# Kernel tuning notes

Measured on AMD Instinct MI355X. Metric: run time of the kernel, lower is better.

## Reference

```python
import jax, jax.numpy as jnp
import numpy as np

EPS = 1e-5  # BatchNorm eps (torch default)
K = 16      # num_neighbors


def _bn(x, gamma, beta, axes):
    # training-mode BatchNorm (biased variance), channel axis = 1
    mu = x.mean(axes, keepdims=True)
    var = x.var(axes, keepdims=True)
    shp = [1] * x.ndim
    shp[1] = -1
    return (x - mu) * jax.lax.rsqrt(var + EPS) * gamma.reshape(shp) + beta.reshape(shp)


def setup_inputs() -> dict:
    key = jax.random.key(0)
    ks = jax.random.split(key, 6)
    B, C, N, E = 4, 3, 4096, 256
    s = lambda k_, shp, fan: jax.random.normal(k_, shp, jnp.float32) * np.float32(1.0 / np.sqrt(fan))
    return {
        "x": jax.random.normal(ks[0], (B, C, N), jnp.float32),
        "g1": jnp.ones((C,), jnp.float32), "b1": jnp.zeros((C,), jnp.float32),
        "W1": s(ks[1], (E, C), C), "bw1": jnp.zeros((E,), jnp.float32),
        "g2a": jnp.ones((C,), jnp.float32), "b2a": jnp.zeros((C,), jnp.float32),
        "W2a": s(ks[2], (E, C), C),
        "g2b": jnp.ones((E,), jnp.float32), "b2b": jnp.zeros((E,), jnp.float32),
        "W2b": s(ks[3], (E, E), E),
        "Wf": s(ks[4], (E, 2 * E), 2 * E), "bf": jnp.zeros((E,), jnp.float32),
    }


def reference(x, g1, b1, W1, bw1, g2a, b2a, W2a, g2b, b2b, W2b, Wf, bf):
    B, C, N = x.shape
    xn = _bn(x, g1, b1, (0, 2))                               # BatchNorm1d
    point_emb = jnp.einsum('ec,bcn->ben', W1, xn) + bw1[None, :, None]  # conv1 (1x1)
    # dist = -||xi - xj||; torch topk(dist, largest=False) picks the K LARGEST
    # distances. Squared distance is monotone in the norm, so top_k on d2 gives
    # identical indices without materializing [B,3,N,N].
    x2 = jnp.sum(xn * xn, axis=1)                             # [B,N]
    d2 = x2[:, :, None] + x2[:, None, :] - 2.0 * jnp.einsum('bcn,bcm->bnm', xn, xn)
    _, idx = jax.lax.top_k(d2, min(K, N))                     # [B,N,K]
    idx = idx[:, :, 1:]                                       # original loop skips index 0
    gathered = jax.vmap(lambda xb, ib: xb[:, ib])(xn, idx)    # [B,C,N,K-1]
    neigh = gathered - xn[:, :, :, None]                      # edge features
    h = _bn(neigh, g2a, b2a, (0, 2, 3))                       # BatchNorm2d(Cin)
    h = jnp.einsum('ec,bcnk->benk', W2a, h)                   # 1x1 conv, no bias
    h = jax.nn.gelu(_bn(h, g2b, b2b, (0, 2, 3)), approximate=False)
    h = jnp.einsum('fe,benk->bfnk', W2b, h)                   # 1x1 conv, no bias
    neigh_emb = h.max(-1)                                     # max over neighbors
    feat = jnp.concatenate([point_emb, neigh_emb], axis=1)    # [B,2E,N]
    return jnp.einsum('of,bfn->bon', Wf, feat) + bf[None, :, None]
```

## Files before the change

### kernel.cpp

```cpp
#include <hip/hip_runtime.h>
#include <float.h>
#include <math.h>

#define EPS 1e-5f
constexpr int B = 4, C = 3, N = 4096, E = 256;
constexpr int KNN = 15;
constexpr int BN_ = B * N;
constexpr int P = 8;
constexpr int SR  = 264;
constexpr int SRF = 520;

typedef short bf8 __attribute__((ext_vector_type(8)));
typedef float f4  __attribute__((ext_vector_type(4)));

static __device__ __forceinline__ unsigned short f2bf(float f) {
    union { float f; unsigned int u; } v; v.f = f;
    unsigned int r = v.u + 0x7FFFu + ((v.u >> 16) & 1u);
    return (unsigned short)(r >> 16);
}
static __device__ __forceinline__ unsigned int pkbf(float a, float b) {
    unsigned int r;
    asm("v_cvt_pk_bf16_f32 %0, %1, %2" : "=v"(r) : "v"(a), "v"(b));
    return r;
}
static __device__ __forceinline__ bf8 ld_bf8(const unsigned short* p) {
    return *(const bf8*)p;
}
static __device__ __forceinline__ float gelu_t(float v) {
    float z = v * fmaf(v * v, 0.07135482f, 1.59576912f);
    float r = __builtin_amdgcn_rcpf(1.f + __expf(z));
    return fmaf(-v, r, v);
}

template <int CTRL>
static __device__ __forceinline__ float dppmax(float x) {
    int xi = __float_as_int(x);
    int yi = __builtin_amdgcn_update_dpp(xi, xi, CTRL, 0xF, 0xF, false);
    return fmaxf(x, __int_as_float(yi));
}
static __device__ __forceinline__ float wave_max_bcast(float x) {
    x = dppmax<0x111>(x);
    x = dppmax<0x112>(x);
    x = dppmax<0x114>(x);
    x = dppmax<0x118>(x);
    x = dppmax<0x142>(x);
    x = dppmax<0x143>(x);
    return __int_as_float(__builtin_amdgcn_readlane(__float_as_int(x), 63));
}

__global__ void bn1_stats(const float* __restrict__ x, float* __restrict__ bn1,
                          float* __restrict__ S9) {
    int c = blockIdx.x, t = threadIdx.x;
    if (c == C) {
        for (int u = t; u < 64 * 9; u += 256) S9[u] = 0.f;
        return;
    }
    float s = 0.f, ss = 0.f;
    for (int i4 = t; i4 < BN_ / 4; i4 += 256) {
        int b = i4 >> 10, n4 = i4 & 1023;
        float4 v = ((const float4*)(x + (b * C + c) * N))[n4];
        s += v.x + v.y + v.z + v.w;
        ss += v.x * v.x + v.y * v.y + v.z * v.z + v.w * v.w;
    }
    __shared__ float rs_[256], rss_[256];
    rs_[t] = s; rss_[t] = ss; __syncthreads();
    for (int w = 128; w > 0; w >>= 1) {
        if (t < w) { rs_[t] += rs_[t + w]; rss_[t] += rss_[t + w]; }
        __syncthreads();
    }
    if (t == 0) {
        float mu = rs_[0] / (float)BN_;
        float var = rss_[0] / (float)BN_ - mu * mu;
        bn1[c] = mu; bn1[3 + c] = rsqrtf(var + EPS);
    }
}

__global__ void compute_xn_cvt(const float* __restrict__ x,
                               const float* __restrict__ g1,
                               const float* __restrict__ b1,
                               const float* __restrict__ bn1,
                               float4* __restrict__ xn4,
                               const float* __restrict__ W2b, const float* __restrict__ Wf,
                               unsigned short* __restrict__ w2b_t, unsigned short* __restrict__ wf_t) {
    int blk = blockIdx.x;
    if (blk < BN_ / 256) {
        int i = blk * 256 + threadIdx.x;
        int b = i >> 12, n = i & (N - 1);
        float v[3];
        #pragma unroll
        for (int c = 0; c < C; c++)
            v[c] = (x[(b * C + c) * N + n] - bn1[c]) * bn1[3 + c] * g1[c] + b1[c];
        float4 o; o.x = v[0]; o.y = v[1]; o.z = v[2];
        o.w = v[0] * v[0] + v[1] * v[1] + v[2] * v[2];
        xn4[i] = o;
        return;
    }
    int ch = (blk - BN_ / 256) * 256 + threadIdx.x;
    if (ch < 8192) {
        int lane = ch & 63, kb = (ch >> 6) & 7, ft16 = ch >> 9;
        int row = ft16 * 16 + (lane & 15);
        int col = kb * 32 + (lane >> 4) * 8;
        #pragma unroll
        for (int j = 0; j < 8; j++)
            w2b_t[ch * 8 + j] = f2bf(W2b[row * 256 + col + j]);
    } else {
        int c2 = ch - 8192;
        int lane = c2 & 63, kb = (c2 >> 6) & 15, ot = c2 >> 10;
        int row = ot * 16 + (lane & 15);
        int col = kb * 32 + (lane >> 4) * 8;
        #pragma unroll
        for (int j = 0; j < 8; j++)
            wf_t[c2 * 8 + j] = f2bf(Wf[row * 512 + col + j]);
    }
}

__global__ void __launch_bounds__(256, 4) knn_kernel(const float4* __restrict__ xn4,
                                                     unsigned short* __restrict__ idxout,
                                                     float* __restrict__ S9) {
    __shared__ float smom[4][15][9];
    __shared__ __align__(16) float4 pts[1024];
    int w = threadIdx.x >> 6, lane = threadIdx.x & 63;
    int i = blockIdx.x * 4 + w;
    int b = i >> 12, n = i & (N - 1);
    const float4* xb = xn4 + b * N;
    float4 qv = xb[n];
    float d[64];
    #pragma unroll
    for (int ch = 0; ch < 4; ch++) {
        if (ch) __syncthreads();
        #pragma unroll
        for (int u = 0; u < 4; u++)
            pts[u * 256 + threadIdx.x] = xb[ch * 1024 + u * 256 + threadIdx.x];
        __syncthreads();
        #pragma unroll
        for (int j = 0; j < 16; j++) {
            float4 p = pts[j * 64 + lane];
            d[ch * 16 + j] = qv.w + p.w - 2.f * (qv.x * p.x + qv.y * p.y + qv.z * p.z);
        }
    }
    float cm[8];
    #pragma unroll
    for (int c = 0; c < 8; c++) {
        float v = d[c * 8];
        #pragma unroll
        for (int s = 1; s < 8; s++) v = fmaxf(v, d[c * 8 + s]);
        cm[c] = v;
    }
    float bv = cm[0];
    #pragma unroll
    for (int c = 1; c < 8; c++) bv = fmaxf(bv, cm[c]);

    int myj = 0;
    for (int r = 0; r < 16; r++) {
        float wv = wave_max_bcast(bv);
        unsigned long long msk = __ballot(bv == wv);
        int wl = __ffsll(msk) - 1;
        int gi = 0;
        if (lane == wl) {
            int cstar = 0; bool got = false;
            #pragma unroll
            for (int c = 0; c < 8; c++) {
                bool h = !got && (cm[c] == bv);
                cstar = h ? c : cstar;
                got = got || h;
            }
            int slot = 0;
            #pragma unroll
            for (int c = 0; c < 8; c++) {
                if (c == cstar) {
                    bool g2 = false;
                    #pragma unroll
                    for (int s = 0; s < 8; s++) {
                        bool h = !g2 && (d[c * 8 + s] == bv);
                        slot = h ? (c * 8 + s) : slot;
                        g2 = g2 || h;
                    }
                    #pragma unroll
                    for (int s = 0; s < 8; s++)
                        d[c * 8 + s] = (c * 8 + s == slot) ? -FLT_MAX : d[c * 8 + s];
                    float v = d[c * 8];
                    #pragma unroll
                    for (int s = 1; s < 8; s++) v = fmaxf(v, d[c * 8 + s]);
                    cm[c] = v;
                }
            }
            bv = cm[0];
            #pragma unroll
            for (int c = 1; c < 8; c++) bv = fmaxf(bv, cm[c]);
            gi = slot * 64 + lane;
        }
        int g = __shfl(gi, wl);
        if (lane == r - 1) myj = g;
    }

    bool act = lane < 15;
    if (act) idxout[i * KNN + lane] = (unsigned short)myj;
    float4 pj = xb[act ? myj : n];
    float v0 = pj.x - qv.x, v1 = pj.y - qv.y, v2 = pj.z - qv.z;
    if (act) {
        float* mm = smom[w][lane];
        mm[0] = v0; mm[1] = v1; mm[2] = v2;
        mm[3] = v0 * v0; mm[4] = v1 * v1; mm[5] = v2 * v2;
        mm[6] = v0 * v1; mm[7] = v0 * v2; mm[8] = v1 * v2;
    }
    __syncthreads();
    int t = threadIdx.x;
    if (t < 36) {
        int wsel = t / 9, j = t % 9;
        float a = 0.f;
        #pragma unroll
        for (int u = 0; u < 15; u++) a += smom[wsel][u][j];
        atomicAdd(&S9[((blockIdx.x * 4 + wsel) & 63) * 9 + j], a);
    }
}

__global__ void finalize_stats(const float* __restrict__ S9,
                               const float* __restrict__ g2a, const float* __restrict__ b2a,
                               const float* __restrict__ W2a,
                               const float* __restrict__ g2b, const float* __restrict__ b2b,
                               float* __restrict__ ab, float4* __restrict__ wsb) {
    const float cnt = (float)(BN_ * KNN);
    __shared__ float S[9];
    __shared__ float alpha[3], beta[3], mu[3], Ehh[3][3];
    int t = threadIdx.x;
    if (t < 9) {
        float a = 0.f;
        for (int u = 0; u < 64; u++) a += S9[u * 9 + t];
        S[t] = a;
    }
    __syncthreads();
    if (t == 0) {
        float m[3];
        float s2[3][3];
        s2[0][0] = S[3]; s2[1][1] = S[4]; s2[2][2] = S[5];
        s2[0][1] = s2[1][0] = S[6]; s2[0][2] = s2[2][0] = S[7]; s2[1][2] = s2[2][1] = S[8];
        for (int c = 0; c < 3; c++) {
            m[c] = S[c] / cnt;
            float var = s2[c][c] / cnt - m[c] * m[c];
            alpha[c] = g2a[c] * rsqrtf(var + EPS);
            beta[c]  = b2a[c] - m[c] * alpha[c];
            mu[c] = m[c];
            ab[c] = alpha[c]; ab[3 + c] = beta[c];
        }
        for (int c = 0; c < 3; c++)
            for (int cc = 0; cc < 3; cc++)
                Ehh[c][cc] = alpha[c] * alpha[cc] * (s2[c][cc] / cnt)
                           + alpha[c] * beta[cc] * m[c]
                           + beta[c] * alpha[cc] * m[cc]
                           + beta[c] * beta[cc];
    }
    __syncthreads();
    int e = t;
    float wv[3], Eh[3];
    for (int c = 0; c < 3; c++) { wv[c] = W2a[e * 3 + c]; Eh[c] = alpha[c] * mu[c] + beta[c]; }
    float mean = wv[0] * Eh[0] + wv[1] * Eh[1] + wv[2] * Eh[2];
    float m2 = 0.f;
    for (int c = 0; c < 3; c++)
        for (int cc = 0; cc < 3; cc++) m2 += wv[c] * wv[cc] * Ehh[c][cc];
    float var = m2 - mean * mean;
    float s = g2b[e] * rsqrtf(var + EPS);
    float4 o;
    o.x = wv[0] * s; o.y = wv[1] * s; o.z = wv[2] * s; o.w = b2b[e] - mean * s;
    wsb[e] = o;
}

__global__ void __launch_bounds__(512, 2) fused_final(
        const float4* __restrict__ xn4, const unsigned short* __restrict__ idx,
        const float* __restrict__ ab,
        const float4* __restrict__ wsb,
        const unsigned short* __restrict__ w2b_t,
        const float* __restrict__ W1, const float* __restrict__ bw1,
        const unsigned short* __restrict__ wf_t, const float* __restrict__ bfv,
        float* __restrict__ out) {
    __shared__ __align__(16) unsigned short hh_bf[2][64 * SR];
    __shared__ __align__(16) unsigned short feat_bf[8 * SRF];
    __shared__ __align__(16) float4 hhat4[P][16];
    int i0 = blockIdx.x * P;
    int t = threadIdx.x;
    int b = i0 >> 12, n0 = i0 & (N - 1);
    const float4* xb = xn4 + b * N;

    int w = t >> 6, lane = t & 63;
    int m = lane & 15, q = lane >> 4;

    auto phaseB = [&](int pg) {
        int ep = t & 127;
        int pq = t >> 7;
        int p  = pg * 4 + pq;
        float4 wA = wsb[2 * ep];
        float4 wB = wsb[2 * ep + 1];
        float g0A = 0.f, g0B = 0.f;
        #pragma unroll
        for (int k = 0; k < KNN; k++) {
            float4 hv = hhat4[p][k];
            float vA = fmaf(wA.x, hv.x, fmaf(wA.y, hv.y, fmaf(wA.z, hv.z, wA.w)));
            float vB = fmaf(wB.x, hv.x, fmaf(wB.y, hv.y, fmaf(wB.z, hv.z, wB.w)));
            float gA = gelu_t(vA), gB = gelu_t(vB);
            *(unsigned int*)&hh_bf[pg][(16 * pq + k) * SR + 2 * ep] = pkbf(gA, gB);
            if (k == 0) { g0A = gA; g0B = gB; }
        }
        *(unsigned int*)&hh_bf[pg][(16 * pq + 15) * SR + 2 * ep] = pkbf(g0A, g0B);
        float4 pv = xb[n0 + p];
        float peA = bw1[2 * ep] + W1[(2 * ep) * 3] * pv.x
                  + W1[(2 * ep) * 3 + 1] * pv.y + W1[(2 * ep) * 3 + 2] * pv.z;
        float peB = bw1[2 * ep + 1] + W1[(2 * ep + 1) * 3] * pv.x
                  + W1[(2 * ep + 1) * 3 + 1] * pv.y + W1[(2 * ep + 1) * 3 + 2] * pv.z;
        *(unsigned int*)&feat_bf[p * SRF + 2 * ep] = pkbf(peA, peB);
    };

    auto phaseC = [&](int pg) {
        bf8 a0[8], a1[8];
        #pragma unroll
        for (int kb = 0; kb < 8; kb++) {
            a0[kb] = ld_bf8(w2b_t + (w * 2 + 0) * 4096 + kb * 512 + lane * 8);
            a1[kb] = ld_bf8(w2b_t + (w * 2 + 1) * 4096 + kb * 512 + lane * 8);
        }
        #pragma unroll 1
        for (int pp = 0; pp < 4; pp++) {
            bf8 hfr[8];
            #pragma unroll
            for (int kb = 0; kb < 8; kb++)
                hfr[kb] = ld_bf8(&hh_bf[pg][(16 * pp + m) * SR + kb * 32 + q * 8]);
            f4 acc0 = {0.f, 0.f, 0.f, 0.f};
            f4 acc1 = {0.f, 0.f, 0.f, 0.f};
            #pragma unroll
            for (int kb = 0; kb < 8; kb++) {
                acc0 = __builtin_amdgcn_mfma_f32_16x16x32_bf16(hfr[kb], a0[kb], acc0, 0, 0, 0);
                acc1 = __builtin_amdgcn_mfma_f32_16x16x32_bf16(hfr[kb], a1[kb], acc1, 0, 0, 0);
            }
            float mx0 = fmaxf(fmaxf(acc0[0], acc0[1]), fmaxf(acc0[2], acc0[3]));
            float mx1 = fmaxf(fmaxf(acc1[0], acc1[1]), fmaxf(acc1[2], acc1[3]));
            mx0 = fmaxf(mx0, __shfl_xor(mx0, 16));
            mx0 = fmaxf(mx0, __shfl_xor(mx0, 32));
            mx1 = fmaxf(mx1, __shfl_xor(mx1, 16));
            mx1 = fmaxf(mx1, __shfl_xor(mx1, 32));
            if (lane < 16) {
                feat_bf[(pg * 4 + pp) * SRF + E + (w * 2 + 0) * 16 + lane] = f2bf(mx0);
                feat_bf[(pg * 4 + pp) * SRF + E + (w * 2 + 1) * 16 + lane] = f2bf(mx1);
            }
        }
    };

    if (t < P * KNN) {
        int p = t / KNN, k = t % KNN;
        int j = idx[(i0 + p) * KNN + k];
        float4 pj = xb[j];
        float4 pn = xb[n0 + p];
        float4 h;
        h.x = ab[0] * (pj.x - pn.x) + ab[3];
        h.y = ab[1] * (pj.y - pn.y) + ab[4];
        h.z = ab[2] * (pj.z - pn.z) + ab[5];
        h.w = 0.f;
        hhat4[p][k] = h;
    }
    __syncthreads();

    phaseB(0);
    __syncthreads();

    phaseB(1);
    phaseC(0);
    __syncthreads();

    f4 accD0 = {0.f, 0.f, 0.f, 0.f};
    f4 accD1 = {0.f, 0.f, 0.f, 0.f};
    phaseC(1);
    {
        bf8 fb8[8];
        #pragma unroll
        for (int k2 = 0; k2 < 8; k2++)
            fb8[k2] = ld_bf8(&feat_bf[(m & 7) * SRF + k2 * 32 + q * 8]);
        #pragma unroll
        for (int k2 = 0; k2 < 8; k2++) {
            bf8 aa = ld_bf8(wf_t + (w * 2 + 0) * 8192 + k2 * 512 + lane * 8);
            accD0 = __builtin_amdgcn_mfma_f32_16x16x32_bf16(aa, fb8[k2], accD0, 0, 0, 0);
        }
        #pragma unroll
        for (int k2 = 0; k2 < 8; k2++) {
            bf8 aa = ld_bf8(wf_t + (w * 2 + 1) * 8192 + k2 * 512 + lane * 8);
            accD1 = __builtin_amdgcn_mfma_f32_16x16x32_bf16(aa, fb8[k2], accD1, 0, 0, 0);
        }
    }
    __syncthreads();

    {
        bf8 fb8[8];
        #pragma unroll
        for (int k2 = 0; k2 < 8; k2++)
            fb8[k2] = ld_bf8(&feat_bf[(m & 7) * SRF + (8 + k2) * 32 + q * 8]);
        #pragma unroll
        for (int k2 = 0; k2 < 8; k2++) {
            bf8 aa = ld_bf8(wf_t + (w * 2 + 0) * 8192 + (8 + k2) * 512 + lane * 8);
            accD0 = __builtin_amdgcn_mfma_f32_16x16x32_bf16(aa, fb8[k2], accD0, 0, 0, 0);
        }
        #pragma unroll
        for (int k2 = 0; k2 < 8; k2++) {
            bf8 aa = ld_bf8(wf_t + (w * 2 + 1) * 8192 + (8 + k2) * 512 + lane * 8);
            accD1 = __builtin_amdgcn_mfma_f32_16x16x32_bf16(aa, fb8[k2], accD1, 0, 0, 0);
        }
        if (m < P) {
            int o0 = (w * 2 + 0) * 16 + 4 * q;
            out[(b * E + o0 + 0) * N + n0 + m] = accD0[0] + bfv[o0 + 0];
            out[(b * E + o0 + 1) * N + n0 + m] = accD0[1] + bfv[o0 + 1];
            out[(b * E + o0 + 2) * N + n0 + m] = accD0[2] + bfv[o0 + 2];
            out[(b * E + o0 + 3) * N + n0 + m] = accD0[3] + bfv[o0 + 3];
            int o1 = (w * 2 + 1) * 16 + 4 * q;
            out[(b * E + o1 + 0) * N + n0 + m] = accD1[0] + bfv[o1 + 0];
            out[(b * E + o1 + 1) * N + n0 + m] = accD1[1] + bfv[o1 + 1];
            out[(b * E + o1 + 2) * N + n0 + m] = accD1[2] + bfv[o1 + 2];
            out[(b * E + o1 + 3) * N + n0 + m] = accD1[3] + bfv[o1 + 3];
        }
    }
}

extern "C" void kernel_launch(void* const* d_in, const int* in_sizes, int n_in,
                              void* d_out, int out_size, void* d_ws, size_t ws_size,
                              hipStream_t stream) {
    (void)in_sizes; (void)n_in; (void)out_size; (void)ws_size;
    const float* x   = (const float*)d_in[0];
    const float* g1  = (const float*)d_in[1];
    const float* b1  = (const float*)d_in[2];
    const float* W1  = (const float*)d_in[3];
    const float* bw1 = (const float*)d_in[4];
    const float* g2a = (const float*)d_in[5];
    const float* b2a = (const float*)d_in[6];
    const float* W2a = (const float*)d_in[7];
    const float* g2b = (const float*)d_in[8];
    const float* b2b = (const float*)d_in[9];
    const float* W2b = (const float*)d_in[10];
    const float* Wf  = (const float*)d_in[11];
    const float* bfv = (const float*)d_in[12];
    float* out = (float*)d_out;

    char* ws = (char*)d_ws;
    size_t off = 0;
    auto alloc = [&](size_t bytes) { size_t o = off; off = (off + bytes + 255) & ~(size_t)255; return o; };
    float4* xn4           = (float4*)(ws + alloc(sizeof(float4) * BN_));
    unsigned short* idx   = (unsigned short*)(ws + alloc(sizeof(unsigned short) * BN_ * KNN));
    float* bn1            = (float*)(ws + alloc(sizeof(float) * 8));
    float* S9             = (float*)(ws + alloc(sizeof(float) * 64 * 9));
    float* ab             = (float*)(ws + alloc(sizeof(float) * 8));
    float4* wsb           = (float4*)(ws + alloc(sizeof(float4) * E));
    unsigned short* w2bt  = (unsigned short*)(ws + alloc(sizeof(unsigned short) * E * E));
    unsigned short* wft   = (unsigned short*)(ws + alloc(sizeof(unsigned short) * E * 2 * E));

    bn1_stats<<<C + 1, 256, 0, stream>>>(x, bn1, S9);
    compute_xn_cvt<<<BN_ / 256 + (8192 + 16384) / 256, 256, 0, stream>>>(
        x, g1, b1, bn1, xn4, W2b, Wf, w2bt, wft);
    knn_kernel<<<BN_ / 4, 256, 0, stream>>>(xn4, idx, S9);
    finalize_stats<<<1, 256, 0, stream>>>(S9, g2a, b2a, W2a, g2b, b2b, ab, wsb);
    fused_final<<<BN_ / P, 512, 0, stream>>>(xn4, idx, ab, wsb, w2bt, W1, bw1, wft, bfv, out);
}
```

Measured before the change: 221.5 us.

## Fold finalize_stats into knn kernel via last-block ticket; drop LDS staging

Removes the separate single-block finalize_stats launch by having the last knn block (chosen with an atomic ticket plus threadfence) compute the BN2 statistics and folded weights. The kNN distance loop now reads points straight from global/L2 instead of staging them in shared memory with barriers, and the winner-lane broadcast uses readlane instead of shfl. This saves a kernel launch and LDS syncs, but the last block serializes the tail work and direct global loads may cost more latency.

Result: slower. 465.7 us (+110.2%).

```diff
diff --git a/kernel.cpp b/kernel.cpp
--- a/kernel.cpp
+++ b/kernel.cpp
@@ -49,10 +49,11 @@
 }
 
 __global__ void bn1_stats(const float* __restrict__ x, float* __restrict__ bn1,
-                          float* __restrict__ S9) {
+                          float* __restrict__ S9, int* __restrict__ ticket) {
     int c = blockIdx.x, t = threadIdx.x;
     if (c == C) {
         for (int u = t; u < 64 * 9; u += 256) S9[u] = 0.f;
+        if (t == 0) ticket[0] = 0;
         return;
     }
     float s = 0.f, ss = 0.f;
@@ -116,9 +117,16 @@
 
 __global__ void __launch_bounds__(256, 4) knn_kernel(const float4* __restrict__ xn4,
                                                      unsigned short* __restrict__ idxout,
-                                                     float* __restrict__ S9) {
+                                                     float* __restrict__ S9,
+                                                     int* __restrict__ ticket,
+                                                     const float* __restrict__ g2a,
+                                                     const float* __restrict__ b2a,
+                                                     const float* __restrict__ W2a,
+                                                     const float* __restrict__ g2b,
+                                                     const float* __restrict__ b2b,
+                                                     float* __restrict__ ab,
+                                                     float4* __restrict__ wsb) {
     __shared__ float smom[4][15][9];
-    __shared__ __align__(16) float4 pts[1024];
     int w = threadIdx.x >> 6, lane = threadIdx.x & 63;
     int i = blockIdx.x * 4 + w;
     int b = i >> 12, n = i & (N - 1);
@@ -126,17 +134,9 @@
     float4 qv = xb[n];
     float d[64];
     #pragma unroll
-    for (int ch = 0; ch < 4; ch++) {
-        if (ch) __syncthreads();
-        #pragma unroll
-        for (int u = 0; u < 4; u++)
-            pts[u * 256 + threadIdx.x] = xb[ch * 1024 + u * 256 + threadIdx.x];
-        __syncthreads();
-        #pragma unroll
-        for (int j = 0; j < 16; j++) {
-            float4 p = pts[j * 64 + lane];
-            d[ch * 16 + j] = qv.w + p.w - 2.f * (qv.x * p.x + qv.y * p.y + qv.z * p.z);
-        }
+    for (int s = 0; s < 64; s++) {
+        float4 p = xb[s * 64 + lane];
+        d[s] = qv.w + p.w - 2.f * (qv.x * p.x + qv.y * p.y + qv.z * p.z);
     }
     float cm[8];
     #pragma unroll
@@ -189,7 +189,7 @@
             for (int c = 1; c < 8; c++) bv = fmaxf(bv, cm[c]);
             gi = slot * 64 + lane;
         }
-        int g = __shfl(gi, wl);
+        int g = __builtin_amdgcn_readlane(gi, wl);
         if (lane == r - 1) myj = g;
     }
 
@@ -212,17 +212,20 @@
         for (int u = 0; u < 15; u++) a += smom[wsel][u][j];
         atomicAdd(&S9[((blockIdx.x * 4 + wsel) & 63) * 9 + j], a);
     }
-}
-
-__global__ void finalize_stats(const float* __restrict__ S9,
-                               const float* __restrict__ g2a, const float* __restrict__ b2a,
-                               const float* __restrict__ W2a,
-                               const float* __restrict__ g2b, const float* __restrict__ b2b,
-                               float* __restrict__ ab, float4* __restrict__ wsb) {
+
+    __threadfence();
+    __shared__ int winner;
+    if (t == 0) {
+        int old = atomicAdd(ticket, 1);
+        winner = (old == (int)gridDim.x - 1) ? 1 : 0;
+    }
+    __syncthreads();
+    if (!winner) return;
+    __threadfence();
+
     const float cnt = (float)(BN_ * KNN);
     __shared__ float S[9];
     __shared__ float alpha[3], beta[3], mu[3], Ehh[3][3];
-    int t = threadIdx.x;
     if (t < 9) {
         float a = 0.f;
         for (int u = 0; u < 64; u++) a += S9[u * 9 + t];
@@ -443,11 +446,12 @@
     float4* wsb           = (float4*)(ws + alloc(sizeof(float4) * E));
     unsigned short* w2bt  = (unsigned short*)(ws + alloc(sizeof(unsigned short) * E * E));
     unsigned short* wft   = (unsigned short*)(ws + alloc(sizeof(unsigned short) * E * 2 * E));
-
-    bn1_stats<<<C + 1, 256, 0, stream>>>(x, bn1, S9);
+    int* ticket           = (int*)(ws + alloc(sizeof(int) * 4));
+
+    bn1_stats<<<C + 1, 256, 0, stream>>>(x, bn1, S9, ticket);
     compute_xn_cvt<<<BN_ / 256 + (8192 + 16384) / 256, 256, 0, stream>>>(
         x, g1, b1, bn1, xn4, W2b, Wf, w2bt, wft);
-    knn_kernel<<<BN_ / 4, 256, 0, stream>>>(xn4, idx, S9);
-    finalize_stats<<<1, 256, 0, stream>>>(S9, g2a, b2a, W2a, g2b, b2b, ab, wsb);
+    knn_kernel<<<BN_ / 4, 256, 0, stream>>>(xn4, idx, S9, ticket,
+                                            g2a, b2a, W2a, g2b, b2b, ab, wsb);
     fused_final<<<BN_ / P, 512, 0, stream>>>(xn4, idx, ab, wsb, w2bt, W1, bw1, wft, bfv, out);
 }
```
